# Optimization experiments

Hardware: AMD Instinct MI355X
Metric: run time of the kernel (lower is better)

Reference implementation:

```python
import jax, jax.numpy as jnp
import numpy as np
from jax import lax

HIDDEN = 1024
HK, HV = 8, 16          # key / value heads (GQA ratio 2)
DK, DV = 64, 64
KSZ = 4                 # causal conv kernel size
KEY_DIM = HK * DK       # 512
VAL_DIM = HV * DV       # 1024
CONV_DIM = 2 * KEY_DIM + VAL_DIM  # 2048
EPS = 1e-6


def setup_inputs() -> dict:
    key = jax.random.key(0)
    ks = jax.random.split(key, 10)
    total = 1536
    w = lambda k, shape, scale: jax.random.normal(k, shape, dtype=jnp.float32) * scale
    return {
        "hidden_states": jax.random.normal(ks[0], (total, HIDDEN), dtype=jnp.float32),
        "W_qkv": w(ks[1], (CONV_DIM, HIDDEN), HIDDEN ** -0.5),
        "W_z": w(ks[2], (VAL_DIM, HIDDEN), HIDDEN ** -0.5),
        "W_b": w(ks[3], (HV, HIDDEN), HIDDEN ** -0.5),
        "W_a": w(ks[4], (HV, HIDDEN), HIDDEN ** -0.5),
        "conv_weight": w(ks[5], (CONV_DIM, KSZ), KSZ ** -0.5),  # depthwise, bias=False
        "dt_bias": jnp.ones((HV,), jnp.float32),
        "A_log": jnp.log(jax.random.uniform(ks[6], (HV,), jnp.float32, 1e-3, 16.0)),
        "norm_weight": jnp.ones((DV,), jnp.float32),
        "W_out": w(ks[7], (HIDDEN, VAL_DIM), VAL_DIM ** -0.5),
        "cu_seqlens": jnp.array([0, 512, 896, 1152, 1536], dtype=jnp.int32),
        "max_seqlen": 512,
    }


def _gated_delta_rule(q, k, v, g, beta):
    """Gated delta rule recurrence.  q,k:(B,S,H,DK) v:(B,S,H,DV) g,beta:(B,S,H).
    S_t = exp(g_t)*S_{t-1};  S_t += beta_t * k_t (v_t - k_t^T S_t);  o_t = q_t^T S_t."""
    qT = q.transpose(1, 0, 2, 3)
    kT = k.transpose(1, 0, 2, 3)
    vT = v.transpose(1, 0, 2, 3)
    gT = g.transpose(1, 0, 2)
    bT = beta.transpose(1, 0, 2)
    B, H, dk, dv = q.shape[0], q.shape[2], q.shape[3], v.shape[3]
    S0 = jnp.zeros((B, H, dk, dv), jnp.float32)

    def step(S, inp):
        qt, kt, vt, gt, bt = inp
        S = S * jnp.exp(gt)[..., None, None]
        kS = jnp.einsum('bhk,bhkv->bhv', kt, S)
        S = S + bt[..., None, None] * kt[..., None] * (vt - kS)[..., None, :]
        ot = jnp.einsum('bhk,bhkv->bhv', qt, S)
        return S, ot

    _, o = lax.scan(step, S0, (qT, kT, vT, gT, bT))
    return o.transpose(1, 0, 2, 3)  # (B,S,H,DV)


def reference(hidden_states, W_qkv, W_z, W_b, W_a, conv_weight, dt_bias, A_log,
              norm_weight, W_out, cu_seqlens, max_seqlen):
    total, hidden = hidden_states.shape
    B = cu_seqlens.shape[0] - 1
    Smax = max_seqlen
    lens = cu_seqlens[1:] - cu_seqlens[:-1]
    pos = jnp.arange(Smax)
    mask = pos[None, :] < lens[:, None]                         # (B,Smax)
    gidx = jnp.clip(cu_seqlens[:-1, None] + pos[None, :], 0, total - 1)
    pad = lambda x: jnp.where(mask[..., None], x[gidx], 0.0)    # packed -> (B,Smax,D)

    # input projections on packed tokens
    mixed = hidden_states @ W_qkv.T    # (total, CONV_DIM)
    z = hidden_states @ W_z.T          # (total, VAL_DIM)
    b = hidden_states @ W_b.T          # (total, HV)
    a = hidden_states @ W_a.T          # (total, HV)

    # causal depthwise conv1d + silu on padded batch
    xm = pad(mixed).transpose(0, 2, 1)                          # (B,C,S)
    y = lax.conv_general_dilated(xm, conv_weight[:, None, :], (1,), [(KSZ - 1, 0)],
                                 feature_group_count=CONV_DIM,
                                 dimension_numbers=('NCH', 'OIH', 'NCH'))
    y = jax.nn.silu(y).transpose(0, 2, 1)                       # (B,S,CONV_DIM)

    q, k, v = jnp.split(y, [KEY_DIM, 2 * KEY_DIM], axis=-1)
    q = q.reshape(B, Smax, HK, DK)
    k = k.reshape(B, Smax, HK, DK)
    v = v.reshape(B, Smax, HV, DV)

    beta = jax.nn.sigmoid(pad(b))                               # (B,S,HV)
    g = -jnp.exp(A_log) * jax.nn.softplus(pad(a) + dt_bias)     # (B,S,HV)

    l2 = lambda x: x * lax.rsqrt(jnp.sum(x * x, -1, keepdims=True) + 1e-6)
    q = l2(q) * (DK ** -0.5)
    k = l2(k)

    rep = HV // HK
    q = jnp.repeat(q, rep, axis=2)
    k = jnp.repeat(k, rep, axis=2)

    o = _gated_delta_rule(q, k, v, g, beta)                     # (B,S,HV,DV)

    # gated RMSNorm over head_v_dim, gate = silu(z)
    zp = pad(z).reshape(B, Smax, HV, DV)
    o = o * lax.rsqrt(jnp.mean(o * o, -1, keepdims=True) + EPS) * norm_weight * jax.nn.silu(zp)

    out = o.reshape(B, Smax, VAL_DIM) @ W_out.T                 # (B,S,hidden)

    # padded -> packed (masked positions scattered to a dummy slot)
    pidx = jnp.where(mask, cu_seqlens[:-1, None] + pos[None, :], total)
    packed = jnp.zeros((total + 1, hidden), out.dtype).at[pidx.reshape(-1)].set(out.reshape(-1, hidden))
    return packed[:total]
```

## Files before the change

kernel.cpp:

```cpp
#include <hip/hip_runtime.h>
#include <hip/hip_bf16.h>
#include <cstddef>

#define TOTAL   1536
#define HIDDEN  1024
#define HK      8
#define HV      16
#define DK      64
#define DV      64
#define KSZ     4
#define KEY_DIM 512
#define VAL_DIM 1024
#define CONV_DIM 2048
#define NSEQ    4
#define MAXCH   27
#define NMIX    3072

typedef _Float16 f16;
typedef __attribute__((ext_vector_type(8))) _Float16 f16x8;
typedef __attribute__((ext_vector_type(4))) _Float16 f16x4;
typedef __attribute__((ext_vector_type(4))) float f32x4;

__device__ __forceinline__ void cstore(float* C, size_t idx, float v) { C[idx] = v; }
__device__ __forceinline__ void cstore(f16* C, size_t idx, float v) { C[idx] = (f16)v; }

__global__ __launch_bounds__(256) void to_f16_all(const float* __restrict__ s0,
                                                  const float* __restrict__ s1,
                                                  const float* __restrict__ s2,
                                                  const float* __restrict__ s3,
                                                  f16* __restrict__ dst) {
    const int b = blockIdx.x;
    const float* src; int sb;
    if (b < 1536)      { src = s0; sb = 0; }
    else if (b < 3584) { src = s1; sb = 1536; }
    else if (b < 4608) { src = s2; sb = 3584; }
    else               { src = s3; sb = 4608; }
    const int local = (b - sb) * 1024 + threadIdx.x * 4;
    const int goff  = b * 1024 + threadIdx.x * 4;
    float4 v = *(const float4*)(src + local);
    f16x4 o = {(f16)v.x, (f16)v.y, (f16)v.z, (f16)v.w};
    *(f16x4*)(dst + goff) = o;
}

#define LDK 72
template <typename TC>
__global__ __launch_bounds__(256) void gemm_mfma(const f16* __restrict__ A,
                                                 const f16* __restrict__ B,
                                                 TC* __restrict__ C,
                                                 int M, int N, int K) {
    __shared__ __align__(16) f16 As[128 * LDK];
    __shared__ __align__(16) f16 Bs[128 * LDK];
    const int tid = threadIdx.x;
    const int m0 = blockIdx.y * 128, n0 = blockIdx.x * 128;
    const int lane = tid & 63, w = tid >> 6;
    const int wm = (w >> 1) * 64, wn = (w & 1) * 64;
    const int fr = lane & 15;
    const int fk = (lane >> 4) * 8;
    const int sr = tid >> 1;
    const int sc = (tid & 1) * 32;

    f32x4 acc[4][4];
#pragma unroll
    for (int i = 0; i < 4; ++i)
#pragma unroll
        for (int j = 0; j < 4; ++j) acc[i][j] = (f32x4){0.f, 0.f, 0.f, 0.f};

    for (int kk = 0; kk < K; kk += 64) {
        const f16* ga = A + (size_t)(m0 + sr) * K + kk + sc;
        const f16* gb = B + (size_t)(n0 + sr) * K + kk + sc;
        uint4 a0 = *(const uint4*)(ga + 0);
        uint4 a1 = *(const uint4*)(ga + 8);
        uint4 a2 = *(const uint4*)(ga + 16);
        uint4 a3 = *(const uint4*)(ga + 24);
        uint4 b0 = *(const uint4*)(gb + 0);
        uint4 b1 = *(const uint4*)(gb + 8);
        uint4 b2 = *(const uint4*)(gb + 16);
        uint4 b3 = *(const uint4*)(gb + 24);
        __syncthreads();
        *(uint4*)&As[sr * LDK + sc + 0]  = a0;
        *(uint4*)&As[sr * LDK + sc + 8]  = a1;
        *(uint4*)&As[sr * LDK + sc + 16] = a2;
        *(uint4*)&As[sr * LDK + sc + 24] = a3;
        *(uint4*)&Bs[sr * LDK + sc + 0]  = b0;
        *(uint4*)&Bs[sr * LDK + sc + 8]  = b1;
        *(uint4*)&Bs[sr * LDK + sc + 16] = b2;
        *(uint4*)&Bs[sr * LDK + sc + 24] = b3;
        __syncthreads();

#pragma unroll
        for (int k2 = 0; k2 < 64; k2 += 32) {
            f16x8 af[4], bfr[4];
#pragma unroll
            for (int i = 0; i < 4; ++i)
                af[i] = *(const f16x8*)&As[(wm + i * 16 + fr) * LDK + k2 + fk];
#pragma unroll
            for (int j = 0; j < 4; ++j)
                bfr[j] = *(const f16x8*)&Bs[(wn + j * 16 + fr) * LDK + k2 + fk];
#pragma unroll
            for (int i = 0; i < 4; ++i)
#pragma unroll
                for (int j = 0; j < 4; ++j)
                    acc[i][j] = __builtin_amdgcn_mfma_f32_16x16x32_f16(
                        af[i], bfr[j], acc[i][j], 0, 0, 0);
        }
    }

    const int er = (lane >> 4) * 4;
#pragma unroll
    for (int i = 0; i < 4; ++i)
#pragma unroll
        for (int j = 0; j < 4; ++j) {
            const int col = n0 + wn + j * 16 + fr;
#pragma unroll
            for (int r = 0; r < 4; ++r) {
                const int row = m0 + wm + i * 16 + er + r;
                cstore(C, (size_t)row * N + col, acc[i][j][r]);
            }
        }
}

__global__ __launch_bounds__(256) void conv_proj(const f16* __restrict__ mixed3,
                                                 const float* __restrict__ cw,
                                                 const int* __restrict__ cu,
                                                 const float* __restrict__ H,
                                                 const float* __restrict__ Wb,
                                                 const float* __restrict__ Wa,
                                                 const float* __restrict__ dtb,
                                                 const float* __restrict__ Alog,
                                                 f16* __restrict__ qb,
                                                 f16* __restrict__ kb,
                                                 f16* __restrict__ vb,
                                                 float* __restrict__ betab,
                                                 float* __restrict__ lgb) {
    const int tok = blockIdx.x;
    const int tid = threadIdx.x;
    const int lane = tid & 63, w = tid >> 6;
    __shared__ float scale[16];

    int b = 0;
    for (int i = 1; i < NSEQ; ++i)
        if (tok >= cu[i]) b = i;
    const int pos = tok - cu[b];

#pragma unroll
    for (int it = 0; it < 8; ++it) {
        const int o = it * 4 + w;
        const float* wrow = (o < 16) ? (Wb + (size_t)o * HIDDEN)
                                     : (Wa + (size_t)(o - 16) * HIDDEN);
        float s = 0.f;
#pragma unroll
        for (int i = 0; i < 4; ++i) {
            float4 a = *(const float4*)&H[(size_t)tok * HIDDEN + i * 256 + lane * 4];
            float4 c = *(const float4*)&wrow[i * 256 + lane * 4];
            s += a.x * c.x + a.y * c.y + a.z * c.z + a.w * c.w;
        }
#pragma unroll
        for (int m = 1; m < 64; m <<= 1) s += __shfl_xor(s, m);
        if (lane == 0) {
            if (o < 16) {
                betab[tok * HV + o] = 1.f / (1.f + expf(-s));
            } else {
                const int hh = o - 16;
                float x = s + dtb[hh];
                float sp = (x > 20.f) ? x : log1pf(expf(x));
                lgb[tok * HV + hh] = -expf(Alog[hh]) * sp;
            }
        }
    }

    float4 yv[2];
#pragma unroll
    for (int it = 0; it < 2; ++it) {
        const int c0 = (tid + it * 256) * 4;
        float wf[4][4];
#pragma unroll
        for (int r = 0; r < 4; ++r) {
            float4 t4 = *(const float4*)&cw[(c0 + r) * 4];
            wf[r][0] = t4.x; wf[r][1] = t4.y; wf[r][2] = t4.z; wf[r][3] = t4.w;
        }
        float4 acc = {0.f, 0.f, 0.f, 0.f};
#pragma unroll
        for (int j = 0; j < KSZ; ++j) {
            const int off = j - (KSZ - 1);
            if (pos + off >= 0) {
                f16x4 xh = *(const f16x4*)&mixed3[(size_t)(tok + off) * NMIX + c0];
                acc.x += wf[0][j] * (float)xh[0]; acc.y += wf[1][j] * (float)xh[1];
                acc.z += wf[2][j] * (float)xh[2]; acc.w += wf[3][j] * (float)xh[3];
            }
        }
        float4 y;
        y.x = acc.x / (1.f + expf(-acc.x));
        y.y = acc.y / (1.f + expf(-acc.y));
        y.z = acc.z / (1.f + expf(-acc.z));
        y.w = acc.w / (1.f + expf(-acc.w));
        yv[it] = y;
        if (it == 0) {
            float p = y.x * y.x + y.y * y.y + y.z * y.z + y.w * y.w;
            p += __shfl_xor(p, 1);
            p += __shfl_xor(p, 2);
            p += __shfl_xor(p, 4);
            p += __shfl_xor(p, 8);
            if ((tid & 15) == 0) scale[tid >> 4] = rsqrtf(p + 1e-6f);
        }
    }
    __syncthreads();

#pragma unroll
    for (int it = 0; it < 2; ++it) {
        const int c0 = (tid + it * 256) * 4;
        float4 y = yv[it];
        if (c0 < KEY_DIM) {
            const float f = scale[c0 >> 6] * 0.125f;
            f16x4 r = {(f16)(y.x * f), (f16)(y.y * f), (f16)(y.z * f), (f16)(y.w * f)};
            *(f16x4*)&qb[(size_t)tok * KEY_DIM + c0] = r;
        } else if (c0 < 2 * KEY_DIM) {
            const float s = scale[c0 >> 6];
            f16x4 r = {(f16)(y.x * s), (f16)(y.y * s), (f16)(y.z * s), (f16)(y.w * s)};
            *(f16x4*)&kb[(size_t)tok * KEY_DIM + (c0 - KEY_DIM)] = r;
        } else {
            f16x4 r = {(f16)y.x, (f16)y.y, (f16)y.z, (f16)y.w};
            *(f16x4*)&vb[(size_t)tok * VAL_DIM + (c0 - 2 * KEY_DIM)] = r;
        }
    }
}

#define SF 72
#define SA 68
__global__ __launch_bounds__(256) void delta_phase1(
        const f16* __restrict__ qb, const f16* __restrict__ kb,
        const f16* __restrict__ vb, const float* __restrict__ lgb,
        const float* __restrict__ betab, const int* __restrict__ cu,
        float* __restrict__ ob, f16* __restrict__ Gg,
        f16* __restrict__ Hg, f16* __restrict__ Zg) {
    const int c = blockIdx.x >> 4;
    const int h = blockIdx.x & 15;
    const int hk = h >> 1;
    int b = -1, base = 0, t1 = 0, cs = 0;
    for (int i = 0; i < NSEQ; ++i) {
        int len = cu[i + 1] - cu[i];
        int nb = (len + 63) >> 6;
        if (b < 0) {
            if (c < cs + nb) { b = i; base = cu[i] + (c - cs) * 64; t1 = cu[i + 1]; }
            else cs += nb;
        }
    }
    if (b < 0) return;
    const size_t slot = (size_t)blockIdx.x * 4096;

    const int tid = threadIdx.x;
    const int lane = tid & 63, w = tid >> 6;
    const int fr = lane & 15;
    const int fk = (lane >> 4) * 8;
    const int er = (lane >> 4) * 4;

    __shared__ __align__(16) f16 Kl[64 * SF];
    __shared__ __align__(16) f16 Ql[64 * SF];
    __shared__ __align__(16) f16 KTd[64 * SF];
    __shared__ __align__(16) f16 Xt[128 * SF];
    __shared__ __align__(16) float Am[64 * SA];
    __shared__ float cl[64], el[64], bl[64], lgl[64], dscl[64];
    f16* Pl = (f16*)Am;

    const int tt = tid >> 2;
    const int tau0 = base + tt;
    const bool valid = tau0 < t1;
    const f16x4 zh4 = {(f16)0.f, (f16)0.f, (f16)0.f, (f16)0.f};
    f16x4 kv[4], qv[4], vv[4];
#pragma unroll
    for (int u4 = 0; u4 < 4; ++u4) {
        const int d = ((tid & 3) << 2) + u4 * 16;
        kv[u4] = valid ? *(const f16x4*)&kb[(size_t)tau0 * KEY_DIM + hk * 64 + d] : zh4;
        qv[u4] = valid ? *(const f16x4*)&qb[(size_t)tau0 * KEY_DIM + hk * 64 + d] : zh4;
        vv[u4] = valid ? *(const f16x4*)&vb[(size_t)tau0 * VAL_DIM + h * 64 + d] : zh4;
    }
    if (tid < 64) {
        const int ta = base + tid;
        const bool v2 = ta < t1;
        lgl[tid] = v2 ? lgb[ta * HV + h] : 0.f;
        bl[tid]  = v2 ? betab[ta * HV + h] : 0.f;
    }
    __syncthreads();

    if (w == 0) {
        float x = lgl[lane];
#pragma unroll
        for (int off = 1; off < 64; off <<= 1) {
            float y = __shfl_up(x, off);
            if (lane >= off) x += y;
        }
        cl[lane] = x;
        el[lane] = expf(x);
        float c63 = __shfl(x, 63);
        dscl[lane] = expf(c63 - x);
    }
    __syncthreads();

    {
        const float bt = bl[tt], bet = bt * el[tt], ds = dscl[tt];
#pragma unroll
        for (int u4 = 0; u4 < 4; ++u4) {
            const int d = ((tid & 3) << 2) + u4 * 16;
            *(f16x4*)&Kl[tt * SF + d] = kv[u4];
            *(f16x4*)&Ql[tt * SF + d] = qv[u4];
#pragma unroll
            for (int e = 0; e < 4; ++e) {
                const float kf = (float)kv[u4][e];
                const float vf = (float)vv[u4][e];
                KTd[(d + e) * SF + tt] = (f16)(kf * ds);
                Xt[(d + e) * SF + tt] = (f16)(bt * vf);
                Xt[(64 + d + e) * SF + tt] = (f16)(bet * kf);
            }
        }
    }
    __syncthreads();

    {
        f16x8 a0 = *(const f16x8*)&Kl[(16 * w + fr) * SF + fk];
        f16x8 a1 = *(const f16x8*)&Kl[(16 * w + fr) * SF + 32 + fk];
#pragma unroll
        for (int j = 0; j < 4; ++j) {
            f16x8 b0 = *(const f16x8*)&Kl[(16 * j + fr) * SF + fk];
            f16x8 b1 = *(const f16x8*)&Kl[(16 * j + fr) * SF + 32 + fk];
            f32x4 acc = {0.f, 0.f, 0.f, 0.f};
            acc = __builtin_amdgcn_mfma_f32_16x16x32_f16(a0, b0, acc, 0, 0, 0);
            acc = __builtin_amdgcn_mfma_f32_16x16x32_f16(a1, b1, acc, 0, 0, 0);
            const int s = 16 * j + fr;
#pragma unroll
            for (int r = 0; r < 4; ++r) {
                const int t = 16 * w + er + r;
                Am[t * SA + s] = (s < t) ? bl[t] * expf(cl[t] - cl[s]) * acc[r] : 0.f;
            }
        }
    }
    __syncthreads();

#pragma unroll
    for (int ib = 0; ib < 4; ++ib) {
        if (tid < 128) {
            float xr[16];
#pragma unroll
            for (int i = 0; i < 16; ++i) {
                const int t = ib * 16 + i;
                float acc = (float)Xt[tid * SF + t];
#pragma unroll
                for (int s = 0; s < 16; ++s)
                    if (s < i) acc -= Am[t * SA + ib * 16 + s] * xr[s];
                xr[i] = acc;
                Xt[tid * SF + t] = (f16)acc;
            }
        }
        __syncthreads();
        if (ib < 3) {
            const int j = tid & 127;
            const int rh = tid >> 7;
            float us[16];
#pragma unroll
            for (int s = 0; s < 16; ++s) us[s] = (float)Xt[j * SF + ib * 16 + s];
            for (int r = (ib + 1) * 16 + rh; r < 64; r += 2) {
                float acc = (float)Xt[j * SF + r];
#pragma unroll
                for (int s = 0; s < 16; ++s)
                    acc -= Am[r * SA + ib * 16 + s] * us[s];
                Xt[j * SF + r] = (f16)acc;
            }
            __syncthreads();
        }
    }

    {
        f16x8 a0 = *(const f16x8*)&Ql[(16 * w + fr) * SF + fk];
        f16x8 a1 = *(const f16x8*)&Ql[(16 * w + fr) * SF + 32 + fk];
        float pv[4][4];
#pragma unroll
        for (int j = 0; j < 4; ++j) {
            f16x8 b0 = *(const f16x8*)&Kl[(16 * j + fr) * SF + fk];
            f16x8 b1 = *(const f16x8*)&Kl[(16 * j + fr) * SF + 32 + fk];
            f32x4 acc = {0.f, 0.f, 0.f, 0.f};
            acc = __builtin_amdgcn_mfma_f32_16x16x32_f16(a0, b0, acc, 0, 0, 0);
            acc = __builtin_amdgcn_mfma_f32_16x16x32_f16(a1, b1, acc, 0, 0, 0);
            const int s = 16 * j + fr;
#pragma unroll
            for (int r = 0; r < 4; ++r) {
                const int t = 16 * w + er + r;
                pv[j][r] = (s <= t) ? expf(cl[t] - cl[s]) * acc[r] : 0.f;
            }
        }
#pragma unroll
        for (int j = 0; j < 4; ++j) {
            const int s = 16 * j + fr;
#pragma unroll
            for (int r = 0; r < 4; ++r)
                Pl[(16 * w + er + r) * SF + s] = (f16)pv[j][r];
        }
    }
    __syncthreads();

    f16x8 pa0 = *(const f16x8*)&Pl[(16 * w + fr) * SF + fk];
    f16x8 pa1 = *(const f16x8*)&Pl[(16 * w + fr) * SF + 32 + fk];
    f16x8 ka0 = *(const f16x8*)&KTd[(16 * w + fr) * SF + fk];
    f16x8 ka1 = *(const f16x8*)&KTd[(16 * w + fr) * SF + 32 + fk];

#pragma unroll
    for (int j = 0; j < 4; ++j) {
        f16x8 b0 = *(const f16x8*)&Xt[(16 * j + fr) * SF + fk];
        f16x8 b1 = *(const f16x8*)&Xt[(16 * j + fr) * SF + 32 + fk];
        f32x4 acc = {0.f, 0.f, 0.f, 0.f};
        acc = __builtin_amdgcn_mfma_f32_16x16x32_f16(pa0, b0, acc, 0, 0, 0);
        acc = __builtin_amdgcn_mfma_f32_16x16x32_f16(pa1, b1, acc, 0, 0, 0);
        const int dv = 16 * j + fr;
#pragma unroll
        for (int r = 0; r < 4; ++r) {
            const int tau = base + 16 * w + er + r;
            if (tau < t1)
                ob[(size_t)tau * VAL_DIM + h * 64 + dv] = acc[r];
        }
    }
#pragma unroll
    for (int j = 0; j < 4; ++j) {
        f16x8 b0 = *(const f16x8*)&Xt[(64 + 16 * j + fr) * SF + fk];
        f16x8 b1 = *(const f16x8*)&Xt[(64 + 16 * j + fr) * SF + 32 + fk];
        f32x4 acc = {0.f, 0.f, 0.f, 0.f};
        acc = __builtin_amdgcn_mfma_f32_16x16x32_f16(pa0, b0, acc, 0, 0, 0);
        acc = __builtin_amdgcn_mfma_f32_16x16x32_f16(pa1, b1, acc, 0, 0, 0);
        const int dk = 16 * j + fr;
#pragma unroll
        for (int r = 0; r < 4; ++r) {
            const int t = 16 * w + er + r;
            Zg[slot + t * 64 + dk] = (f16)(el[t] * (float)Ql[t * SF + dk] - acc[r]);
        }
    }
#pragma unroll
    for (int j = 0; j < 4; ++j) {
        f16x8 b0 = *(const f16x8*)&Xt[(16 * j + fr) * SF + fk];
        f16x8 b1 = *(const f16x8*)&Xt[(16 * j + fr) * SF + 32 + fk];
        f32x4 acc = {0.f, 0.f, 0.f, 0.f};
        acc = __builtin_amdgcn_mfma_f32_16x16x32_f16(ka0, b0, acc, 0, 0, 0);
        acc = __builtin_amdgcn_mfma_f32_16x16x32_f16(ka1, b1, acc, 0, 0, 0);
        const int dv = 16 * j + fr;
#pragma unroll
        for (int r = 0; r < 4; ++r) {
            const int dk = 16 * w + er + r;
            Hg[slot + dk * 64 + dv] = (f16)acc[r];
        }
    }
    const float e63v = el[63];
#pragma unroll
    for (int j = 0; j < 4; ++j) {
        f16x8 b0 = *(const f16x8*)&Xt[(64 + 16 * j + fr) * SF + fk];
        f16x8 b1 = *(const f16x8*)&Xt[(64 + 16 * j + fr) * SF + 32 + fk];
        f32x4 acc = {0.f, 0.f, 0.f, 0.f};
        acc = __builtin_amdgcn_mfma_f32_16x16x32_f16(ka0, b0, acc, 0, 0, 0);
        acc = __builtin_amdgcn_mfma_f32_16x16x32_f16(ka1, b1, acc, 0, 0, 0);
        const int dk2 = 16 * j + fr;
#pragma unroll
        for (int r = 0; r < 4; ++r) {
            const int dk = 16 * w + er + r;
            Gg[slot + dk * 64 + dk2] = (f16)(((dk == dk2) ? e63v : 0.f) - acc[r]);
        }
    }
}

__global__ __launch_bounds__(256) void delta_scan(
        const int* __restrict__ cu, const f16* __restrict__ Gg,
        const f16* __restrict__ Hg, f16* __restrict__ Sc) {
    const int b = blockIdx.x >> 4, h = blockIdx.x & 15;
    const int tid = threadIdx.x;
    const int lane = tid & 63, w = tid >> 6;
    const int fr = lane & 15;
    const int fk = (lane >> 4) * 8;
    const int er = (lane >> 4) * 4;

    __shared__ __align__(16) f16 Sl[64 * SF];
    for (int i = tid; i < 64 * SF; i += 256) Sl[i] = (f16)0.f;

    int cs = 0;
    for (int i = 0; i < b; ++i) cs += ((cu[i + 1] - cu[i]) + 63) >> 6;
    const int t0 = cu[b], t1 = cu[b + 1];
    const int nb = (t1 - t0 + 63) >> 6;

    for (int ci = 0; ci < nb; ++ci) {
        const size_t slot = (size_t)((cs + ci) * 16 + h) * 4096;
        __syncthreads();

        {
            const int r = tid >> 2;
            const int c0 = (tid & 3) * 16;
            uint4 s0 = *(const uint4*)&Sl[r * SF + c0];
            uint4 s1 = *(const uint4*)&Sl[r * SF + c0 + 8];
            *(uint4*)&Sc[slot + r * 64 + c0] = s0;
            *(uint4*)&Sc[slot + r * 64 + c0 + 8] = s1;
        }

        f16x8 ga0 = *(const f16x8*)&Gg[slot + (16 * w + fr) * 64 + fk];
        f16x8 ga1 = *(const f16x8*)&Gg[slot + (16 * w + fr) * 64 + 32 + fk];
        f16x8 sb[4][2];
        f32x4 acc[4];
#pragma unroll
        for (int j = 0; j < 4; ++j) {
            sb[j][0] = *(const f16x8*)&Sl[(16 * j + fr) * SF + fk];
            sb[j][1] = *(const f16x8*)&Sl[(16 * j + fr) * SF + 32 + fk];
            const int dv = 16 * j + fr;
#pragma unroll
            for (int r = 0; r < 4; ++r)
                acc[j][r] = (float)Hg[slot + (16 * w + er + r) * 64 + dv];
        }
        __syncthreads();
#pragma unroll
        for (int j = 0; j < 4; ++j) {
            acc[j] = __builtin_amdgcn_mfma_f32_16x16x32_f16(ga0, sb[j][0], acc[j], 0, 0, 0);
            acc[j] = __builtin_amdgcn_mfma_f32_16x16x32_f16(ga1, sb[j][1], acc[j], 0, 0, 0);
            const int dv = 16 * j + fr;
#pragma unroll
            for (int r = 0; r < 4; ++r)
                Sl[dv * SF + 16 * w + er + r] = (f16)acc[j][r];
        }
    }
}

__global__ __launch_bounds__(256) void delta_out(
        const int* __restrict__ cu, const f16* __restrict__ Zg,
        const f16* __restrict__ Sc, const float* __restrict__ ob,
        const f16* __restrict__ mixed3, const float* __restrict__ nw,
        f16* __restrict__ obf) {
    const int c = blockIdx.x >> 4;
    const int h = blockIdx.x & 15;
    int b = -1, base = 0, t1 = 0, cs = 0;
    for (int i = 0; i < NSEQ; ++i) {
        int len = cu[i + 1] - cu[i];
        int nbc = (len + 63) >> 6;
        if (b < 0) {
            if (c < cs + nbc) { b = i; base = cu[i] + (c - cs) * 64; t1 = cu[i + 1]; }
            else cs += nbc;
        }
    }
    if (b < 0) return;
    const size_t slot = (size_t)blockIdx.x * 4096;

    const int tid = threadIdx.x;
    const int lane = tid & 63, w = tid >> 6;
    const int fr = lane & 15;
    const int fk = (lane >> 4) * 8;
    const int er = (lane >> 4) * 4;

    f16x8 za0 = *(const f16x8*)&Zg[slot + (16 * w + fr) * 64 + fk];
    f16x8 za1 = *(const f16x8*)&Zg[slot + (16 * w + fr) * 64 + 32 + fk];

    float oacc[4][4];
#pragma unroll
    for (int j = 0; j < 4; ++j) {
        f16x8 b0 = *(const f16x8*)&Sc[slot + (16 * j + fr) * 64 + fk];
        f16x8 b1 = *(const f16x8*)&Sc[slot + (16 * j + fr) * 64 + 32 + fk];
        f32x4 acc = {0.f, 0.f, 0.f, 0.f};
        acc = __builtin_amdgcn_mfma_f32_16x16x32_f16(za0, b0, acc, 0, 0, 0);
        acc = __builtin_amdgcn_mfma_f32_16x16x32_f16(za1, b1, acc, 0, 0, 0);
        const int dv = 16 * j + fr;
#pragma unroll
        for (int r = 0; r < 4; ++r) {
            const int tau = base + 16 * w + er + r;
            oacc[j][r] = (tau < t1)
                ? ob[(size_t)tau * VAL_DIM + h * 64 + dv] + acc[r] : 0.f;
        }
    }
    float ss[4];
#pragma unroll
    for (int r = 0; r < 4; ++r) {
        ss[r] = oacc[0][r] * oacc[0][r] + oacc[1][r] * oacc[1][r]
              + oacc[2][r] * oacc[2][r] + oacc[3][r] * oacc[3][r];
#pragma unroll
        for (int m = 1; m < 16; m <<= 1) ss[r] += __shfl_xor(ss[r], m);
    }
#pragma unroll
    for (int r = 0; r < 4; ++r) {
        const int tau = base + 16 * w + er + r;
        if (tau < t1) {
            const float rms = rsqrtf(ss[r] * (1.f / 64.f) + 1e-6f);
#pragma unroll
            for (int j = 0; j < 4; ++j) {
                const int col = 16 * j + fr;
                const float z = (float)mixed3[(size_t)tau * NMIX + 2048 + h * 64 + col];
                const float sz = z / (1.f + expf(-z));
                obf[(size_t)tau * VAL_DIM + h * 64 + col] =
                    (f16)(oacc[j][r] * rms * nw[col] * sz);
            }
        }
    }
}

extern "C" void kernel_launch(void* const* d_in, const int* in_sizes, int n_in,
                              void* d_out, int out_size, void* d_ws, size_t ws_size,
                              hipStream_t stream) {
    const float* H    = (const float*)d_in[0];
    const float* Wqkv = (const float*)d_in[1];
    const float* Wz   = (const float*)d_in[2];
    const float* Wb   = (const float*)d_in[3];
    const float* Wa   = (const float*)d_in[4];
    const float* cwt  = (const float*)d_in[5];
    const float* dtb  = (const float*)d_in[6];
    const float* Alog = (const float*)d_in[7];
    const float* nw   = (const float*)d_in[8];
    const float* Wout = (const float*)d_in[9];
    const int*   cu   = (const int*)d_in[10];
    float* out = (float*)d_out;

    f16* mixed3 = (f16*)d_ws;
    float* obuf  = (float*)(mixed3 + (size_t)TOTAL * NMIX);
    float* lgbuf = obuf + (size_t)TOTAL * VAL_DIM;
    float* bbuf  = lgbuf + (size_t)TOTAL * HV;
    f16* Hb    = (f16*)(bbuf + (size_t)TOTAL * HV);
    f16* Wqkvb = Hb + (size_t)TOTAL * HIDDEN;
    f16* Wzb   = Wqkvb + (size_t)CONV_DIM * HIDDEN;
    f16* Woutb = Wzb + (size_t)VAL_DIM * HIDDEN;
    f16* qbuf  = Woutb + (size_t)HIDDEN * VAL_DIM;
    f16* kbuf  = qbuf + (size_t)TOTAL * KEY_DIM;
    f16* vbuf  = kbuf + (size_t)TOTAL * KEY_DIM;
    f16* obf   = vbuf + (size_t)TOTAL * VAL_DIM;
    f16* Gg    = obf + (size_t)TOTAL * VAL_DIM;
    f16* Hg    = Gg + (size_t)MAXCH * 16 * 4096;
    f16* Zg    = Hg + (size_t)MAXCH * 16 * 4096;
    f16* Scg   = Zg + (size_t)MAXCH * 16 * 4096;

    to_f16_all<<<5632, 256, 0, stream>>>(H, Wqkv, Wz, Wout, Hb);

    gemm_mfma<f16><<<dim3(NMIX / 128, TOTAL / 128), 256, 0, stream>>>(
        Hb, Wqkvb, mixed3, TOTAL, NMIX, HIDDEN);
    conv_proj<<<TOTAL, 256, 0, stream>>>(mixed3, cwt, cu, H, Wb, Wa, dtb, Alog,
                                         qbuf, kbuf, vbuf, bbuf, lgbuf);
    delta_phase1<<<MAXCH * 16, 256, 0, stream>>>(qbuf, kbuf, vbuf, lgbuf, bbuf,
                                                 cu, obuf, Gg, Hg, Zg);
    delta_scan<<<NSEQ * HV, 256, 0, stream>>>(cu, Gg, Hg, Scg);
    delta_out<<<MAXCH * 16, 256, 0, stream>>>(cu, Zg, Scg, obuf, mixed3, nw, obf);
    gemm_mfma<float><<<dim3(HIDDEN / 128, TOTAL / 128), 256, 0, stream>>>(
        obf, Woutb, out, TOTAL, HIDDEN, VAL_DIM);
}
```

Before: 205.2 us.

## Double-buffer shared-memory tiles in MFMA GEMM to overlap loads with compute

Converts the GEMM main loop to a two-stage software pipeline. Global loads for the next K tile are issued into registers before the MFMA work on the current tile, then written to the alternate LDS buffer, which leaves one barrier per iteration instead of two. This is meant to hide global load latency behind the matrix math. It doubles LDS use per block (about 72 KB), which may lower occupancy, and keeps more live registers.

After: 199.8 us. 1.03x faster.

```diff
diff --git a/kernel.cpp b/kernel.cpp
--- a/kernel.cpp
+++ b/kernel.cpp
@@ -48,8 +48,8 @@
                                                  const f16* __restrict__ B,
                                                  TC* __restrict__ C,
                                                  int M, int N, int K) {
-    __shared__ __align__(16) f16 As[128 * LDK];
-    __shared__ __align__(16) f16 Bs[128 * LDK];
+    __shared__ __align__(16) f16 As[2][128 * LDK];
+    __shared__ __align__(16) f16 Bs[2][128 * LDK];
     const int tid = threadIdx.x;
     const int m0 = blockIdx.y * 128, n0 = blockIdx.x * 128;
     const int lane = tid & 63, w = tid >> 6;
@@ -65,9 +65,10 @@
 #pragma unroll
         for (int j = 0; j < 4; ++j) acc[i][j] = (f32x4){0.f, 0.f, 0.f, 0.f};
 
-    for (int kk = 0; kk < K; kk += 64) {
-        const f16* ga = A + (size_t)(m0 + sr) * K + kk + sc;
-        const f16* gb = B + (size_t)(n0 + sr) * K + kk + sc;
+    const f16* ga = A + (size_t)(m0 + sr) * K + sc;
+    const f16* gb = B + (size_t)(n0 + sr) * K + sc;
+
+    {
         uint4 a0 = *(const uint4*)(ga + 0);
         uint4 a1 = *(const uint4*)(ga + 8);
         uint4 a2 = *(const uint4*)(ga + 16);
@@ -76,32 +77,61 @@
         uint4 b1 = *(const uint4*)(gb + 8);
         uint4 b2 = *(const uint4*)(gb + 16);
         uint4 b3 = *(const uint4*)(gb + 24);
-        __syncthreads();
-        *(uint4*)&As[sr * LDK + sc + 0]  = a0;
-        *(uint4*)&As[sr * LDK + sc + 8]  = a1;
-        *(uint4*)&As[sr * LDK + sc + 16] = a2;
-        *(uint4*)&As[sr * LDK + sc + 24] = a3;
-        *(uint4*)&Bs[sr * LDK + sc + 0]  = b0;
-        *(uint4*)&Bs[sr * LDK + sc + 8]  = b1;
-        *(uint4*)&Bs[sr * LDK + sc + 16] = b2;
-        *(uint4*)&Bs[sr * LDK + sc + 24] = b3;
-        __syncthreads();
+        *(uint4*)&As[0][sr * LDK + sc + 0]  = a0;
+        *(uint4*)&As[0][sr * LDK + sc + 8]  = a1;
+        *(uint4*)&As[0][sr * LDK + sc + 16] = a2;
+        *(uint4*)&As[0][sr * LDK + sc + 24] = a3;
+        *(uint4*)&Bs[0][sr * LDK + sc + 0]  = b0;
+        *(uint4*)&Bs[0][sr * LDK + sc + 8]  = b1;
+        *(uint4*)&Bs[0][sr * LDK + sc + 16] = b2;
+        *(uint4*)&Bs[0][sr * LDK + sc + 24] = b3;
+    }
+    __syncthreads();
+
+    int cur = 0;
+    for (int kk = 64; kk <= K; kk += 64) {
+        const bool more = kk < K;
+        uint4 a0, a1, a2, a3, b0, b1, b2, b3;
+        if (more) {
+            a0 = *(const uint4*)(ga + kk + 0);
+            a1 = *(const uint4*)(ga + kk + 8);
+            a2 = *(const uint4*)(ga + kk + 16);
+            a3 = *(const uint4*)(ga + kk + 24);
+            b0 = *(const uint4*)(gb + kk + 0);
+            b1 = *(const uint4*)(gb + kk + 8);
+            b2 = *(const uint4*)(gb + kk + 16);
+            b3 = *(const uint4*)(gb + kk + 24);
+        }
 
 #pragma unroll
         for (int k2 = 0; k2 < 64; k2 += 32) {
             f16x8 af[4], bfr[4];
 #pragma unroll
             for (int i = 0; i < 4; ++i)
-                af[i] = *(const f16x8*)&As[(wm + i * 16 + fr) * LDK + k2 + fk];
+                af[i] = *(const f16x8*)&As[cur][(wm + i * 16 + fr) * LDK + k2 + fk];
 #pragma unroll
             for (int j = 0; j < 4; ++j)
-                bfr[j] = *(const f16x8*)&Bs[(wn + j * 16 + fr) * LDK + k2 + fk];
+                bfr[j] = *(const f16x8*)&Bs[cur][(wn + j * 16 + fr) * LDK + k2 + fk];
 #pragma unroll
             for (int i = 0; i < 4; ++i)
 #pragma unroll
                 for (int j = 0; j < 4; ++j)
                     acc[i][j] = __builtin_amdgcn_mfma_f32_16x16x32_f16(
                         af[i], bfr[j], acc[i][j], 0, 0, 0);
+        }
+
+        if (more) {
+            const int nxt = cur ^ 1;
+            *(uint4*)&As[nxt][sr * LDK + sc + 0]  = a0;
+            *(uint4*)&As[nxt][sr * LDK + sc + 8]  = a1;
+            *(uint4*)&As[nxt][sr * LDK + sc + 16] = a2;
+            *(uint4*)&As[nxt][sr * LDK + sc + 24] = a3;
+            *(uint4*)&Bs[nxt][sr * LDK + sc + 0]  = b0;
+            *(uint4*)&Bs[nxt][sr * LDK + sc + 8]  = b1;
+            *(uint4*)&Bs[nxt][sr * LDK + sc + 16] = b2;
+            *(uint4*)&Bs[nxt][sr * LDK + sc + 24] = b3;
+            __syncthreads();
+            cur = nxt;
         }
     }
 
```
